# Kernel tuning notes

Hardware: AMD Instinct MI355X
Metric: run time of the kernel (lower is better)

## Reference

```python
import jax, jax.numpy as jnp
import numpy as np

D, H, CTX, FFN, KS = 512, 8, 128, 2048, 31
B, S = 4, 4096
EPS = 1e-5

def _ln(x, g, b):
    m = jnp.mean(x, -1, keepdims=True)
    v = jnp.mean((x - m) ** 2, -1, keepdims=True)
    return (x - m) * jax.lax.rsqrt(v + EPS) * g + b

def _ffn(x, g, b, w1, b1, w2, b2):
    h = jax.nn.gelu(_ln(x, g, b) @ w1 + b1, approximate=False)
    return h @ w2 + b2

def _local_attn(x, wq, bq, wk, bk, wv, bv, wo, bo, rel_bias):
    Bz, Sz, Dz = x.shape
    Hd = Dz // H
    def proj(w, bias):
        return (x @ w + bias).reshape(Bz, Sz, H, Hd).transpose(0, 2, 1, 3)
    q, k, v = proj(wq, bq), proj(wk, bk), proj(wv, bv)
    nb = Sz // CTX
    def win(t):  # gather 3 neighboring blocks per query block -> [B,H,nb,3*CTX,Hd]
        tp = jnp.pad(t, ((0, 0), (0, 0), (CTX, CTX), (0, 0)))
        tb = tp.reshape(Bz, H, nb + 2, CTX, Hd)
        return jnp.concatenate([tb[:, :, :-2], tb[:, :, 1:-1], tb[:, :, 2:]], axis=3)
    kw, vw = win(k), win(v)
    qb = q.reshape(Bz, H, nb, CTX, Hd)
    scores = jnp.einsum('bhnqd,bhnkd->bhnqk', qb, kw) * (Hd ** -0.5)
    qi = jnp.arange(CTX)[:, None]
    kj = jnp.arange(3 * CTX)[None, :]
    rel = kj - CTX - qi  # [CTX, 3*CTX], relative position j - i
    scores = scores + rel_bias[:, jnp.clip(rel + CTX, 0, 2 * CTX)][None, :, None]
    j_glob = jnp.arange(nb)[:, None, None] * CTX - CTX + kj[None]  # [nb,1,3*CTX]
    valid = (jnp.abs(rel) <= CTX)[None] & (j_glob >= 0) & (j_glob < Sz)  # [nb,CTX,3*CTX]
    scores = jnp.where(valid[None, None], scores, -jnp.inf)
    w = jax.nn.softmax(scores, axis=-1)
    out = jnp.einsum('bhnqk,bhnkd->bhnqd', w, vw).reshape(Bz, H, Sz, Hd)
    out = out.transpose(0, 2, 1, 3).reshape(Bz, Sz, Dz)
    return out @ wo + bo

def _conv_mod(x, g, b, pw1_w, pw1_b, dw_w, dw_b, bn_g, bn_b, bn_m, bn_v, pw2_w, pw2_b):
    h = _ln(x, g, b) @ pw1_w + pw1_b  # [B,S,2D]
    a, gate = jnp.split(h, 2, axis=-1)
    h = a * jax.nn.sigmoid(gate)  # GLU
    hc = h.transpose(0, 2, 1)  # [B,D,S]
    hc = jax.lax.conv_general_dilated(
        hc, dw_w, (1,), [(KS // 2, KS // 2)],
        feature_group_count=D, dimension_numbers=('NCH', 'OIH', 'NCH')) + dw_b[None, :, None]
    hc = (hc - bn_m[None, :, None]) * jax.lax.rsqrt(bn_v[None, :, None] + EPS) * bn_g[None, :, None] + bn_b[None, :, None]
    hc = hc * jax.nn.sigmoid(hc)  # SiLU
    return hc.transpose(0, 2, 1) @ pw2_w + pw2_b

def setup_inputs() -> dict:
    key = jax.random.key(0)
    ks = iter(jax.random.split(key, 40))
    def w(*shape, s=0.02):
        return jax.random.normal(next(ks), shape, dtype=jnp.float32) * s
    d = {}
    d['x'] = jax.random.normal(next(ks), (B, S, D), dtype=jnp.float32)
    for p in ('ff1', 'ff2'):
        d[p + '_ln_g'] = jnp.ones((D,)); d[p + '_ln_b'] = jnp.zeros((D,))
        d[p + '_w1'] = w(D, FFN); d[p + '_b1'] = jnp.zeros((FFN,))
        d[p + '_w2'] = w(FFN, D); d[p + '_b2'] = jnp.zeros((D,))
    d['attn_ln_g'] = jnp.ones((D,)); d['attn_ln_b'] = jnp.zeros((D,))
    for p in ('wq', 'wk', 'wv', 'wo'):
        d[p] = w(D, D)
    for p in ('bq', 'bk', 'bv', 'bo'):
        d[p] = jnp.zeros((D,))
    d['rel_bias'] = w(H, 2 * CTX + 1)
    d['conv_ln_g'] = jnp.ones((D,)); d['conv_ln_b'] = jnp.zeros((D,))
    d['pw1_w'] = w(D, 2 * D); d['pw1_b'] = jnp.zeros((2 * D,))
    d['dw_w'] = w(D, 1, KS); d['dw_b'] = jnp.zeros((D,))
    d['bn_g'] = jnp.ones((D,)); d['bn_b'] = jnp.zeros((D,))
    d['bn_m'] = jnp.zeros((D,)); d['bn_v'] = jnp.ones((D,))
    d['pw2_w'] = w(D, D); d['pw2_b'] = jnp.zeros((D,))
    d['fin_ln_g'] = jnp.ones((D,)); d['fin_ln_b'] = jnp.zeros((D,))
    return d

def reference(x, ff1_ln_g, ff1_ln_b, ff1_w1, ff1_b1, ff1_w2, ff1_b2,
              ff2_ln_g, ff2_ln_b, ff2_w1, ff2_b1, ff2_w2, ff2_b2,
              attn_ln_g, attn_ln_b, wq, wk, wv, wo, bq, bk, bv, bo, rel_bias,
              conv_ln_g, conv_ln_b, pw1_w, pw1_b, dw_w, dw_b,
              bn_g, bn_b, bn_m, bn_v, pw2_w, pw2_b, fin_ln_g, fin_ln_b):
    x = x + 0.5 * _ffn(x, ff1_ln_g, ff1_ln_b, ff1_w1, ff1_b1, ff1_w2, ff1_b2)
    x = x + _local_attn(_ln(x, attn_ln_g, attn_ln_b), wq, bq, wk, bk, wv, bv, wo, bo, rel_bias)
    x = x + _conv_mod(x, conv_ln_g, conv_ln_b, pw1_w, pw1_b, dw_w, dw_b,
                      bn_g, bn_b, bn_m, bn_v, pw2_w, pw2_b)
    x = x + 0.5 * _ffn(x, ff2_ln_g, ff2_ln_b, ff2_w1, ff2_b1, ff2_w2, ff2_b2)
    return _ln(x, fin_ln_g, fin_ln_b)
```

## Files before the change

### kernel.cpp

```cpp
#include <hip/hip_runtime.h>
#include <hip/hip_bf16.h>
#include <math.h>


using bf16 = __hip_bfloat16;
typedef __bf16 bf16x8_t __attribute__((ext_vector_type(8)));
typedef float f32x4_t __attribute__((ext_vector_type(4)));

static __device__ __forceinline__ float bf2f(bf16 v) { return __bfloat162float(v); }
static __device__ __forceinline__ bf16 f2bf(float v) { return __float2bfloat16(v); }

#define GLOAD_LDS16(g, l)                                                            \
    __builtin_amdgcn_global_load_lds((const __attribute__((address_space(1))) void*)(g), \
                                     (__attribute__((address_space(3))) void*)(l), 16, 0, 0)

struct WSrcs { const float* s[10]; };
__global__ __launch_bounds__(256) void k_wconv(WSrcs srcs, bf16* __restrict__ wc) {
    const int start[11] = {0, 1024, 2048, 3072, 4096, 4352, 4608, 4864, 5120, 5632, 5888};
    const int Ks[10]    = {512, 2048, 512, 2048, 512, 512, 512, 512, 512, 512};
    const int Ns[10]    = {2048, 512, 2048, 512, 512, 512, 512, 512, 1024, 512};
    const int doff[10]  = {0, 1048576, 2097152, 3145728, 4194304, 4456448, 4718592, 4980736, 5242880, 5767168};
    int id = blockIdx.x, seg = 0;
#pragma unroll
    for (int i = 1; i < 10; ++i) seg += (id >= start[i]);
    int lid = id - start[seg];
    int K = Ks[seg], N = Ns[seg];
    int nbx = N >> 5;
    int bx = lid % nbx, by = lid / nbx;
    int nb = bx * 32, kb = by * 32;
    const float* in = srcs.s[seg];
    bf16* out = wc + doff[seg];
    bool inter = (seg == 8);
    __shared__ float t[32][33];
    int c = threadIdx.x & 31, r0 = threadIdx.x >> 5;
#pragma unroll
    for (int i = 0; i < 4; ++i)
        t[r0 + i * 8][c] = in[(size_t)(kb + r0 + i * 8) * N + nb + c];
    __syncthreads();
#pragma unroll
    for (int i = 0; i < 4; ++i) {
        int n = nb + r0 + i * 8;
        int orow = inter ? ((n < 512) ? 2 * n : 2 * (n - 512) + 1) : n;
        out[(size_t)orow * K + kb + c] = f2bf(t[c][r0 + i * 8]);
    }
}

template <bool BF16OUT>
__global__ __launch_bounds__(256) void k_ln(const float* __restrict__ x, const float* __restrict__ g,
                                            const float* __restrict__ b, void* __restrict__ outp) {
    int row = blockIdx.x * 4 + (threadIdx.x >> 6), t = threadIdx.x & 63;
    const float* xr = x + (size_t)row * 512 + t * 8;
    float4 v0 = *(const float4*)xr;
    float4 v1 = *(const float4*)(xr + 4);
    float vals[8] = {v0.x, v0.y, v0.z, v0.w, v1.x, v1.y, v1.z, v1.w};
    float s = 0.f, ss = 0.f;
#pragma unroll
    for (int j = 0; j < 8; ++j) { s += vals[j]; ss += vals[j] * vals[j]; }
#pragma unroll
    for (int o = 32; o > 0; o >>= 1) { s += __shfl_xor(s, o, 64); ss += __shfl_xor(ss, o, 64); }
    float mean = s * (1.0f / 512.0f);
    float var  = ss * (1.0f / 512.0f) - mean * mean;
    float r = rsqrtf(var + 1e-5f);
    float4 g0 = *(const float4*)(g + t * 8);
    float4 g1 = *(const float4*)(g + t * 8 + 4);
    float4 b0 = *(const float4*)(b + t * 8);
    float4 b1 = *(const float4*)(b + t * 8 + 4);
    float gv[8] = {g0.x, g0.y, g0.z, g0.w, g1.x, g1.y, g1.z, g1.w};
    float bv[8] = {b0.x, b0.y, b0.z, b0.w, b1.x, b1.y, b1.z, b1.w};
    float ov[8];
#pragma unroll
    for (int j = 0; j < 8; ++j) ov[j] = (vals[j] - mean) * r * gv[j] + bv[j];
    if (BF16OUT) {
        union { uint4 u; bf16 h[8]; } oo;
#pragma unroll
        for (int j = 0; j < 8; ++j) oo.h[j] = f2bf(ov[j]);
        *(uint4*)((bf16*)outp + (size_t)row * 512 + t * 8) = oo.u;
    } else {
        float* op = (float*)outp + (size_t)row * 512 + t * 8;
        *(float4*)op = make_float4(ov[0], ov[1], ov[2], ov[3]);
        *(float4*)(op + 4) = make_float4(ov[4], ov[5], ov[6], ov[7]);
    }
}

template <int MODE, int TN>
__global__ __launch_bounds__(256) void k_gemm(const bf16* __restrict__ A, const bf16* __restrict__ Bt,
                                              const float* __restrict__ bias, void* __restrict__ outp,
                                              int M, int N, int K, float scale,
                                              const float* __restrict__ b2, const float* __restrict__ b3,
                                              const float* __restrict__ resid, int nbx) {
    constexpr int NT = TN / 32;
    __shared__ __align__(16) bf16 As[2][128 * 32];
    __shared__ __align__(16) bf16 Bs[2][TN * 32];
    int id = blockIdx.x;
    int xcd = id & 7, slot = id >> 3;
    int nbyg = (gridDim.x / nbx) >> 3;
    int bxi = slot % nbx;
    int byi = slot / nbx + xcd * nbyg;
    int bn = bxi * TN, bm = byi * 128;
    int tid = threadIdx.x, w = tid >> 6, l = tid & 63;
    int l15 = l & 15, quad = l >> 4;
    int wm = (w >> 1) * 64, wn = (w & 1) * (TN / 2);
    f32x4_t acc[4][NT] = {};
    const int brows = TN / 4;
    const bf16* ag = A + (size_t)(bm + w * 32 + (l >> 2)) * K + (l & 3) * 8;
    const bf16* bg = Bt + (size_t)(bn + w * brows + (l >> 2)) * K + (l & 3) * 8;

    auto stage = [&](int buf, int k0) {
        bf16* asl = As[buf] + w * 32 * 32;
        bf16* bsl = Bs[buf] + w * brows * 32;
#pragma unroll
        for (int j = 0; j < 2; ++j)
            GLOAD_LDS16(ag + (size_t)j * 16 * K + k0, asl + j * 16 * 32);
#pragma unroll
        for (int j = 0; j < TN / 64; ++j)
            GLOAD_LDS16(bg + (size_t)j * 16 * K + k0, bsl + j * 16 * 32);
    };

    const int nt = K >> 5;
    stage(0, 0);
    int cur = 0;
    for (int t = 0; t < nt; ++t) {
        __syncthreads();
        if (t + 1 < nt) stage(cur ^ 1, (t + 1) * 32);
        bf16x8_t af[4], bfr[NT];
#pragma unroll
        for (int tm = 0; tm < 4; ++tm)
            af[tm] = *(const bf16x8_t*)(As[cur] + (wm + tm * 16 + l15) * 32 + quad * 8);
#pragma unroll
        for (int tn = 0; tn < NT; ++tn)
            bfr[tn] = *(const bf16x8_t*)(Bs[cur] + (wn + tn * 16 + l15) * 32 + quad * 8);
#pragma unroll
        for (int tm = 0; tm < 4; ++tm)
#pragma unroll
            for (int tn = 0; tn < NT; ++tn)
                acc[tm][tn] = __builtin_amdgcn_mfma_f32_16x16x32_bf16(af[tm], bfr[tn], acc[tm][tn], 0, 0, 0);
        cur ^= 1;
    }
    __syncthreads();
    float* tb = (float*)(&As[0][0]) + w * 576;
#pragma unroll
    for (int tm = 0; tm < 4; ++tm)
#pragma unroll
        for (int cp = 0; cp < NT / 2; ++cp) {
#pragma unroll
            for (int j = 0; j < 2; ++j)
#pragma unroll
                for (int r = 0; r < 4; ++r)
                    tb[(quad * 4 + r) * 36 + j * 16 + l15] = acc[tm][2 * cp + j][r];
            int lr = l >> 2, lc = (l & 3) * 8;
            float v[8];
#pragma unroll
            for (int i = 0; i < 8; ++i) v[i] = tb[lr * 36 + lc + i];
            int gr = bm + wm + tm * 16 + lr;
            int gc = bn + wn + cp * 32 + lc;
            if (MODE == 0 || MODE == 1) {
                union { uint4 u; bf16 h[8]; } oo;
#pragma unroll
                for (int i = 0; i < 8; ++i) {
                    float vv = v[i] + bias[gc + i];
                    if (MODE == 1) {
                        float z = vv * (1.5957691f + 0.07135481f * vv * vv);
                        vv = vv / (1.f + __expf(-z));
                    }
                    oo.h[i] = f2bf(vv);
                }
                *(uint4*)((bf16*)outp + (size_t)gr * N + gc) = oo.u;
            } else if (MODE == 2) {
                size_t ix = (size_t)gr * N + gc;
                float4 r0 = *(const float4*)(resid + ix);
                float4 r1 = *(const float4*)(resid + ix + 4);
                float rr[8] = {r0.x, r0.y, r0.z, r0.w, r1.x, r1.y, r1.z, r1.w};
                float o[8];
#pragma unroll
                for (int i = 0; i < 8; ++i) o[i] = rr[i] + scale * (v[i] + bias[gc + i]);
                *(float4*)((float*)outp + ix) = make_float4(o[0], o[1], o[2], o[3]);
                *(float4*)((float*)outp + ix + 4) = make_float4(o[4], o[5], o[6], o[7]);
            } else if (MODE == 3) {
                const float* bp = (gc < 512) ? bias : (gc < 1024 ? b2 : b3);
                int cc = gc & 511;
                union { uint4 u; bf16 h[8]; } oo;
#pragma unroll
                for (int i = 0; i < 8; ++i) oo.h[i] = f2bf(v[i] + bp[cc + i]);
                bf16* ob = (bf16*)outp + (size_t)(gc >> 9) * 8388608;
                *(uint4*)(ob + (size_t)gr * 512 + cc) = oo.u;
            } else {
                union { ushort4 u; bf16 h[4]; } oo;
#pragma unroll
                for (int p = 0; p < 4; ++p) {
                    int ic = gc + 2 * p;
                    float a = v[2 * p] + bias[ic >> 1];
                    float gt = v[2 * p + 1] + bias[(ic >> 1) + 512];
                    oo.h[p] = f2bf(a / (1.f + __expf(-gt)));
                }
                *(ushort4*)((bf16*)outp + (size_t)gr * (N >> 1) + (gc >> 1)) = oo.u;
            }
        }
}

__global__ __launch_bounds__(256) void k_attn(const bf16* __restrict__ q, const bf16* __restrict__ k,
                                              const bf16* __restrict__ v, const float* __restrict__ rel_bias,
                                              bf16* __restrict__ out) {
    __shared__ __align__(16) bf16 Qs[128][72];
    __shared__ __align__(16) bf16 Ks[64][72];
    __shared__ __align__(16) bf16 Vt[64][72];
    __shared__ __align__(16) bf16 Pb[4][32][72];
    __shared__ float relb[257];
    int blk = blockIdx.x;
    int n = blk & 31, h = (blk >> 5) & 7, b = blk >> 8;
    int tid = threadIdx.x, w = tid >> 6, lane = tid & 63;
    int l15 = lane & 15, quad = lane >> 4;
    for (int i = tid; i < 257; i += 256) relb[i] = rel_bias[h * 257 + i];
    {
        const bf16* qg = q + (size_t)(b * 4096 + n * 128) * 512 + h * 64;
#pragma unroll
        for (int i = 0; i < 4; ++i) {
            int slot = tid + 256 * i;
            int row = slot >> 3, col = (slot & 7) * 8;
            *(uint4*)&Qs[row][col] = *(const uint4*)(qg + (size_t)row * 512 + col);
        }
    }
    float m_run[2][4], l_run[2][4];
#pragma unroll
    for (int qt = 0; qt < 2; ++qt)
#pragma unroll
        for (int r = 0; r < 4; ++r) { m_run[qt][r] = -1e30f; l_run[qt][r] = 0.f; }
    f32x4_t Oacc[2][4] = {};
    int kv0 = n * 128 - 128;
    for (int ch = 0; ch < 6; ++ch) {
        int kst = kv0 + ch * 64;
        if (kst < 0 || kst >= 4096) continue;
        __syncthreads();
        {
#pragma unroll
            for (int i = 0; i < 2; ++i) {
                int slot = tid + 256 * i;
                int row = slot >> 3, col = (slot & 7) * 8;
                *(uint4*)&Ks[row][col] = *(const uint4*)(k + (size_t)(b * 4096 + kst + row) * 512 + h * 64 + col);
            }
        }
        {
            int key = tid >> 2, c0 = (tid & 3) * 16;
            union { uint4 u[2]; bf16 hh[16]; } tv;
            const bf16* vg = v + (size_t)(b * 4096 + kst + key) * 512 + h * 64 + c0;
            tv.u[0] = *(const uint4*)vg;
            tv.u[1] = *(const uint4*)(vg + 8);
#pragma unroll
            for (int j = 0; j < 16; ++j) Vt[c0 + j][key] = tv.hh[j];
        }
        __syncthreads();
        bf16x8_t qf[2][2];
#pragma unroll
        for (int qt = 0; qt < 2; ++qt)
#pragma unroll
            for (int ks = 0; ks < 2; ++ks)
                qf[qt][ks] = *(const bf16x8_t*)&Qs[w * 32 + qt * 16 + l15][ks * 32 + quad * 8];
        float sc[2][4][4];
#pragma unroll
        for (int qt = 0; qt < 2; ++qt)
#pragma unroll
            for (int nt = 0; nt < 4; ++nt) {
                f32x4_t a = {};
#pragma unroll
                for (int ks = 0; ks < 2; ++ks) {
                    bf16x8_t kf = *(const bf16x8_t*)&Ks[nt * 16 + l15][ks * 32 + quad * 8];
                    a = __builtin_amdgcn_mfma_f32_16x16x32_bf16(qf[qt][ks], kf, a, 0, 0, 0);
                }
#pragma unroll
                for (int r = 0; r < 4; ++r) sc[qt][nt][r] = a[r];
            }
#pragma unroll
        for (int qt = 0; qt < 2; ++qt)
#pragma unroll
            for (int nt = 0; nt < 4; ++nt)
#pragma unroll
                for (int r = 0; r < 4; ++r) {
                    int qrow = w * 32 + qt * 16 + quad * 4 + r;
                    int rel = ch * 64 + nt * 16 + l15 - 128 - qrow;
                    int idx = rel + 128; idx = idx < 0 ? 0 : (idx > 256 ? 256 : idx);
                    float s = sc[qt][nt][r] * 0.125f + relb[idx];
                    sc[qt][nt][r] = (rel >= -128 && rel <= 128) ? s : -INFINITY;
                }
        float al[2][4];
#pragma unroll
        for (int qt = 0; qt < 2; ++qt)
#pragma unroll
            for (int r = 0; r < 4; ++r) {
                float mx = fmaxf(fmaxf(sc[qt][0][r], sc[qt][1][r]), fmaxf(sc[qt][2][r], sc[qt][3][r]));
#pragma unroll
                for (int mk = 1; mk <= 8; mk <<= 1) mx = fmaxf(mx, __shfl_xor(mx, mk, 64));
                float mn = fmaxf(m_run[qt][r], mx);
                float a = __expf(m_run[qt][r] - mn);
                float ps = 0.f;
#pragma unroll
                for (int nt = 0; nt < 4; ++nt) {
                    float p = __expf(sc[qt][nt][r] - mn);
                    sc[qt][nt][r] = p;
                    ps += p;
                }
#pragma unroll
                for (int mk = 1; mk <= 8; mk <<= 1) ps += __shfl_xor(ps, mk, 64);
                l_run[qt][r] = l_run[qt][r] * a + ps;
                m_run[qt][r] = mn;
                al[qt][r] = a;
            }
#pragma unroll
        for (int qt = 0; qt < 2; ++qt)
#pragma unroll
            for (int nt = 0; nt < 4; ++nt)
#pragma unroll
                for (int r = 0; r < 4; ++r)
                    Pb[w][qt * 16 + quad * 4 + r][nt * 16 + l15] = f2bf(sc[qt][nt][r]);
        __syncthreads();
#pragma unroll
        for (int qt = 0; qt < 2; ++qt) {
#pragma unroll
            for (int dt = 0; dt < 4; ++dt)
#pragma unroll
                for (int r = 0; r < 4; ++r)
                    Oacc[qt][dt][r] *= al[qt][r];
            bf16x8_t pf[2];
#pragma unroll
            for (int ks = 0; ks < 2; ++ks)
                pf[ks] = *(const bf16x8_t*)&Pb[w][qt * 16 + l15][ks * 32 + quad * 8];
#pragma unroll
            for (int dt = 0; dt < 4; ++dt) {
                f32x4_t a = Oacc[qt][dt];
#pragma unroll
                for (int ks = 0; ks < 2; ++ks) {
                    bf16x8_t vf = *(const bf16x8_t*)&Vt[dt * 16 + l15][ks * 32 + quad * 8];
                    a = __builtin_amdgcn_mfma_f32_16x16x32_bf16(pf[ks], vf, a, 0, 0, 0);
                }
                Oacc[qt][dt] = a;
            }
        }
    }
#pragma unroll
    for (int qt = 0; qt < 2; ++qt)
#pragma unroll
        for (int r = 0; r < 4; ++r) {
            float inv = 1.f / l_run[qt][r];
            int row = n * 128 + w * 32 + qt * 16 + quad * 4 + r;
#pragma unroll
            for (int dt = 0; dt < 4; ++dt)
                out[(size_t)(b * 4096 + row) * 512 + h * 64 + dt * 16 + l15] = f2bf(Oacc[qt][dt][r] * inv);
        }
}

__global__ __launch_bounds__(256) void k_conv(const bf16* __restrict__ in, const float* __restrict__ w,
                                              const float* __restrict__ wb, const float* __restrict__ bg,
                                              const float* __restrict__ bb2, const float* __restrict__ bm,
                                              const float* __restrict__ bvv, bf16* __restrict__ out) {
    __shared__ float wl[64 * 31];
    int d0 = blockIdx.x * 64, s0 = blockIdx.y * 64, b = blockIdx.z;
    for (int i = threadIdx.x; i < 64 * 31; i += 256) wl[i] = w[d0 * 31 + i];
    __syncthreads();
    int dl = threadIdx.x & 63, chunk = threadIdx.x >> 6;
    int d = d0 + dl;
    int s00 = s0 + chunk * 16;
    float wr[31];
#pragma unroll
    for (int t = 0; t < 31; ++t) wr[t] = wl[dl * 31 + t];
    float xw[46];
    const bf16* base = in + (size_t)(b * 4096) * 512 + d;
#pragma unroll
    for (int i = 0; i < 46; ++i) {
        int s = s00 - 15 + i;
        xw[i] = (s >= 0 && s < 4096) ? bf2f(base[(size_t)s * 512]) : 0.f;
    }
    float scv = bg[d] * rsqrtf(bvv[d] + 1e-5f);
    float wbd = wb[d], bmd = bm[d], bbd = bb2[d];
    bf16* op = out + (size_t)(b * 4096 + s00) * 512 + d;
#pragma unroll
    for (int j = 0; j < 16; ++j) {
        float acc = 0.f;
#pragma unroll
        for (int t = 0; t < 31; ++t) acc += wr[t] * xw[j + t];
        acc += wbd;
        acc = (acc - bmd) * scv + bbd;
        acc = acc / (1.f + __expf(-acc));
        op[(size_t)j * 512] = f2bf(acc);
    }
}

extern "C" void kernel_launch(void* const* d_in, const int* in_sizes, int n_in,
                              void* d_out, int out_size, void* d_ws, size_t ws_size,
                              hipStream_t stream) {
    (void)in_sizes; (void)n_in; (void)out_size; (void)ws_size;
    const float* x = (const float*)d_in[0];
    char* ws = (char*)d_ws;
    float* xf   = (float*)ws;
    bf16* ln_bf = (bf16*)(ws + 33554432);
    bf16* h_bf  = (bf16*)(ws + 50331648);
    bf16* g_bf  = (bf16*)(ws + 117440512);
    bf16* t_bf  = (bf16*)(ws + 134217728);
    bf16* wc    = (bf16*)(ws + 150994944);
    bf16 *qb = h_bf;
    bf16* w_f11 = wc;
    bf16* w_f12 = wc + 1048576;
    bf16* w_f21 = wc + 2097152;
    bf16* w_f22 = wc + 3145728;
    bf16* w_q   = wc + 4194304;
    bf16* w_o   = wc + 4980736;
    bf16* w_p1  = wc + 5242880;
    bf16* w_p2  = wc + 5767168;

    WSrcs srcs;
    srcs.s[0] = (const float*)d_in[3];  srcs.s[1] = (const float*)d_in[5];
    srcs.s[2] = (const float*)d_in[9];  srcs.s[3] = (const float*)d_in[11];
    srcs.s[4] = (const float*)d_in[15]; srcs.s[5] = (const float*)d_in[16];
    srcs.s[6] = (const float*)d_in[17]; srcs.s[7] = (const float*)d_in[18];
    srcs.s[8] = (const float*)d_in[26]; srcs.s[9] = (const float*)d_in[34];
    k_wconv<<<5888, 256, 0, stream>>>(srcs, wc);

    k_ln<true><<<4096, 256, 0, stream>>>(x, (const float*)d_in[1], (const float*)d_in[2], ln_bf);
    k_gemm<1, 128><<<2048, 256, 0, stream>>>(ln_bf, w_f11, (const float*)d_in[4], h_bf, 16384, 2048, 512, 0.f, nullptr, nullptr, nullptr, 16);
    k_gemm<2, 64><<<1024, 256, 0, stream>>>(h_bf, w_f12, (const float*)d_in[6], xf, 16384, 512, 2048, 0.5f, nullptr, nullptr, x, 8);
    k_ln<true><<<4096, 256, 0, stream>>>(xf, (const float*)d_in[13], (const float*)d_in[14], ln_bf);
    k_gemm<3, 64><<<3072, 256, 0, stream>>>(ln_bf, w_q, (const float*)d_in[19], qb, 16384, 1536, 512, 0.f,
                                            (const float*)d_in[20], (const float*)d_in[21], nullptr, 24);
    k_attn<<<1024, 256, 0, stream>>>(qb, qb + 8388608, qb + 16777216, (const float*)d_in[23], t_bf);
    k_gemm<2, 64><<<1024, 256, 0, stream>>>(t_bf, w_o, (const float*)d_in[22], xf, 16384, 512, 512, 1.0f, nullptr, nullptr, xf, 8);
    k_ln<true><<<4096, 256, 0, stream>>>(xf, (const float*)d_in[24], (const float*)d_in[25], ln_bf);
    k_gemm<5, 64><<<2048, 256, 0, stream>>>(ln_bf, w_p1, (const float*)d_in[27], g_bf, 16384, 1024, 512, 0.f, nullptr, nullptr, nullptr, 16);
    k_conv<<<dim3(8, 64, 4), 256, 0, stream>>>(g_bf, (const float*)d_in[28], (const float*)d_in[29], (const float*)d_in[30],
                                               (const float*)d_in[31], (const float*)d_in[32], (const float*)d_in[33], t_bf);
    k_gemm<2, 64><<<1024, 256, 0, stream>>>(t_bf, w_p2, (const float*)d_in[35], xf, 16384, 512, 512, 1.0f, nullptr, nullptr, xf, 8);
    k_ln<true><<<4096, 256, 0, stream>>>(xf, (const float*)d_in[7], (const float*)d_in[8], ln_bf);
    k_gemm<1, 128><<<2048, 256, 0, stream>>>(ln_bf, w_f21, (const float*)d_in[10], h_bf, 16384, 2048, 512, 0.f, nullptr, nullptr, nullptr, 16);
    k_gemm<2, 64><<<1024, 256, 0, stream>>>(h_bf, w_f22, (const float*)d_in[12], xf, 16384, 512, 2048, 0.5f, nullptr, nullptr, xf, 8);
    k_ln<false><<<4096, 256, 0, stream>>>(xf, (const float*)d_in[36], (const float*)d_in[37], d_out);
}
```

Baseline: 634.8 us.

## Register-prefetch K/V chunks, keep Q in registers, drop redundant barrier in attention

```diff
diff --git a/kernel.cpp b/kernel.cpp
--- a/kernel.cpp
+++ b/kernel.cpp
@@ -200,7 +200,6 @@
 __global__ __launch_bounds__(256) void k_attn(const bf16* __restrict__ q, const bf16* __restrict__ k,
                                               const bf16* __restrict__ v, const float* __restrict__ rel_bias,
                                               bf16* __restrict__ out) {
-    __shared__ __align__(16) bf16 Qs[128][72];
     __shared__ __align__(16) bf16 Ks[64][72];
     __shared__ __align__(16) bf16 Vt[64][72];
     __shared__ __align__(16) bf16 Pb[4][32][72];
@@ -210,15 +209,18 @@
     int tid = threadIdx.x, w = tid >> 6, lane = tid & 63;
     int l15 = lane & 15, quad = lane >> 4;
     for (int i = tid; i < 257; i += 256) relb[i] = rel_bias[h * 257 + i];
-    {
-        const bf16* qg = q + (size_t)(b * 4096 + n * 128) * 512 + h * 64;
-#pragma unroll
-        for (int i = 0; i < 4; ++i) {
-            int slot = tid + 256 * i;
-            int row = slot >> 3, col = (slot & 7) * 8;
-            *(uint4*)&Qs[row][col] = *(const uint4*)(qg + (size_t)row * 512 + col);
+    bf16x8_t qf[2][2];
+#pragma unroll
+    for (int qt = 0; qt < 2; ++qt)
+#pragma unroll
+        for (int ks = 0; ks < 2; ++ks) {
+            const bf16* qg = q + (size_t)(b * 4096 + n * 128 + w * 32 + qt * 16 + l15) * 512
+                               + h * 64 + ks * 32 + quad * 8;
+            bf16x8_t f = *(const bf16x8_t*)qg;
+#pragma unroll
+            for (int j = 0; j < 8; ++j) f[j] = (__bf16)(0.125f * (float)f[j]);
+            qf[qt][ks] = f;
         }
-    }
     float m_run[2][4], l_run[2][4];
 #pragma unroll
     for (int qt = 0; qt < 2; ++qt)
@@ -226,34 +228,29 @@
         for (int r = 0; r < 4; ++r) { m_run[qt][r] = -1e30f; l_run[qt][r] = 0.f; }
     f32x4_t Oacc[2][4] = {};
     int kv0 = n * 128 - 128;
-    for (int ch = 0; ch < 6; ++ch) {
-        int kst = kv0 + ch * 64;
-        if (kst < 0 || kst >= 4096) continue;
+    int lo = (n == 0) ? 2 : 0;
+    int hi = (n == 31) ? 4 : 6;
+    int krow = tid >> 3, kcol = (tid & 7) * 8;
+    int vkey = tid >> 2, vc0 = (tid & 3) * 16;
+    uint4 kr0, kr1;
+    union { uint4 u[2]; bf16 hh[16]; } vr;
+    auto loadKV = [&](int kst) {
+        const bf16* kg = k + (size_t)(b * 4096 + kst + krow) * 512 + h * 64 + kcol;
+        kr0 = *(const uint4*)kg;
+        kr1 = *(const uint4*)(kg + (size_t)32 * 512);
+        const bf16* vg = v + (size_t)(b * 4096 + kst + vkey) * 512 + h * 64 + vc0;
+        vr.u[0] = *(const uint4*)vg;
+        vr.u[1] = *(const uint4*)(vg + 8);
+    };
+    loadKV(kv0 + lo * 64);
+    for (int ch = lo; ch < hi; ++ch) {
         __syncthreads();
-        {
-#pragma unroll
-            for (int i = 0; i < 2; ++i) {
-                int slot = tid + 256 * i;
-                int row = slot >> 3, col = (slot & 7) * 8;
-                *(uint4*)&Ks[row][col] = *(const uint4*)(k + (size_t)(b * 4096 + kst + row) * 512 + h * 64 + col);
-            }
-        }
-        {
-            int key = tid >> 2, c0 = (tid & 3) * 16;
-            union { uint4 u[2]; bf16 hh[16]; } tv;
-            const bf16* vg = v + (size_t)(b * 4096 + kst + key) * 512 + h * 64 + c0;
-            tv.u[0] = *(const uint4*)vg;
-            tv.u[1] = *(const uint4*)(vg + 8);
-#pragma unroll
-            for (int j = 0; j < 16; ++j) Vt[c0 + j][key] = tv.hh[j];
-        }
+        *(uint4*)&Ks[krow][kcol] = kr0;
+        *(uint4*)&Ks[krow + 32][kcol] = kr1;
+#pragma unroll
+        for (int j = 0; j < 16; ++j) Vt[vc0 + j][vkey] = vr.hh[j];
+        if (ch + 1 < hi) loadKV(kv0 + (ch + 1) * 64);
         __syncthreads();
-        bf16x8_t qf[2][2];
-#pragma unroll
-        for (int qt = 0; qt < 2; ++qt)
-#pragma unroll
-            for (int ks = 0; ks < 2; ++ks)
-                qf[qt][ks] = *(const bf16x8_t*)&Qs[w * 32 + qt * 16 + l15][ks * 32 + quad * 8];
         float sc[2][4][4];
 #pragma unroll
         for (int qt = 0; qt < 2; ++qt)
@@ -277,7 +274,7 @@
                     int qrow = w * 32 + qt * 16 + quad * 4 + r;
                     int rel = ch * 64 + nt * 16 + l15 - 128 - qrow;
                     int idx = rel + 128; idx = idx < 0 ? 0 : (idx > 256 ? 256 : idx);
-                    float s = sc[qt][nt][r] * 0.125f + relb[idx];
+                    float s = sc[qt][nt][r] + relb[idx];
                     sc[qt][nt][r] = (rel >= -128 && rel <= 128) ? s : -INFINITY;
                 }
         float al[2][4];
@@ -310,7 +307,6 @@
 #pragma unroll
                 for (int r = 0; r < 4; ++r)
                     Pb[w][qt * 16 + quad * 4 + r][nt * 16 + l15] = f2bf(sc[qt][nt][r]);
-        __syncthreads();
 #pragma unroll
         for (int qt = 0; qt < 2; ++qt) {
 #pragma unroll
```

After: 640.9 us. No clear change (+1.0%).
